# Kernel tuning notes

Hardware: AMD Instinct MI355X
Metric: run time of the kernel (lower is better)

The kernel has to match this reference:

```python
import jax, jax.numpy as jnp
import numpy as np

K_FRAC = 0.5  # matches init kwarg k


def setup_inputs() -> dict:
    key = jax.random.key(0)
    g = jax.random.normal(key, (16, 2048, 2048), dtype=jnp.float32)
    return {"g": g}


def reference(g):
    # k = int(N * k_frac): number of SMALLEST entries per row to zero out
    N = g.shape[-1]
    k = int(N * K_FRAC)
    g2 = g.reshape(-1, N)                       # [R, N]
    # indices of the k smallest values per row (topk of -g)
    _, idx = jax.lax.top_k(-g2, k)              # [R, k] int32
    rows = jnp.arange(g2.shape[0])[:, None]     # [R, 1]
    t = g2.at[rows, idx].set(0.0)               # scatter zeros at bottom-k positions
    return t.reshape(g.shape)
```

## Files before the change

### kernel.cpp

```cpp
#include <hip/hip_runtime.h>

#define ROW_N 2048
#define ROW_K 1024
#define NSUB 4
#define HPAD 264
#define WH   (NSUB * HPAD)
#define WSTRIDE (WH + 4)

__device__ __forceinline__ void wfence() {
    asm volatile("s_waitcnt lgkmcnt(0)" ::: "memory");
}

__device__ __forceinline__ unsigned f2key(float x) {
    unsigned u = __float_as_uint(x);
    return u ^ ((unsigned)((int)u >> 31) | 0x80000000u);
}
__device__ __forceinline__ float key2f(unsigned k) {
    unsigned u = (k & 0x80000000u) ? (k ^ 0x80000000u) : ~k;
    return __uint_as_float(u);
}

__global__ __launch_bounds__(256)
void ktakes_kernel(const float* __restrict__ g, float* __restrict__ out) {
    const int tid  = threadIdx.x;
    const int wave = tid >> 6;
    const int lane = tid & 63;
    const int row  = blockIdx.x * 4 + wave;

    __shared__ unsigned H[4 * WSTRIDE];
    unsigned* hw   = H + wave * WSTRIDE;
    unsigned* hsub = hw + (lane & (NSUB - 1)) * HPAD;

    const float4* g4 = reinterpret_cast<const float4*>(g + (size_t)row * ROW_N);
    float4*       o4 = reinterpret_cast<float4*>(out + (size_t)row * ROW_N);

    unsigned k[32];
#pragma unroll
    for (int j = 0; j < 8; ++j) {
        float4 v = g4[j * 64 + lane];
        k[4*j+0] = f2key(v.x); k[4*j+1] = f2key(v.y);
        k[4*j+2] = f2key(v.z); k[4*j+3] = f2key(v.w);
    }

    unsigned prefix = 0;
    int rank = ROW_K - 1;
    int cnteq = 0;

#pragma unroll
    for (int r = 0; r < 4; ++r) {
        const int shift = 24 - 8 * r;

#pragma unroll
        for (int i = 0; i < 17; ++i) {
            int idx = i * 64 + lane;
            if (idx < WH) hw[idx] = 0;
        }
        wfence();

        if (r == 0) {
#pragma unroll
            for (int c = 0; c < 32; ++c)
                atomicAdd(&hsub[k[c] >> 24], 1u);
        } else {
            const int hs = shift + 8;
#pragma unroll
            for (int c = 0; c < 32; ++c)
                if (((k[c] ^ prefix) >> hs) == 0)
                    atomicAdd(&hsub[(k[c] >> shift) & 255u], 1u);
        }
        wfence();

        uint4 h0 = *reinterpret_cast<const uint4*>(&hw[0 * HPAD + 4 * lane]);
        uint4 h1 = *reinterpret_cast<const uint4*>(&hw[1 * HPAD + 4 * lane]);
        uint4 h2 = *reinterpret_cast<const uint4*>(&hw[2 * HPAD + 4 * lane]);
        uint4 h3 = *reinterpret_cast<const uint4*>(&hw[3 * HPAD + 4 * lane]);
        unsigned b0 = h0.x + h1.x + h2.x + h3.x;
        unsigned b1 = h0.y + h1.y + h2.y + h3.y;
        unsigned b2 = h0.z + h1.z + h2.z + h3.z;
        unsigned b3 = h0.w + h1.w + h2.w + h3.w;
        wfence();

        unsigned s4 = b0 + b1 + b2 + b3;
        unsigned incl = s4;
#pragma unroll
        for (int off = 1; off < 64; off <<= 1) {
            unsigned n = __shfl_up(incl, off, 64);
            if (lane >= off) incl += n;
        }
        int excl = (int)(incl - s4);
        bool found = (rank >= excl) && (rank < (int)incl);

        int rr = rank - excl;
        unsigned d = 4 * lane;
        unsigned beq = b0;
        if (found) {
            if (rr >= (int)b0) { rr -= (int)b0; d++; beq = b1;
                if (rr >= (int)b1) { rr -= (int)b1; d++; beq = b2;
                    if (rr >= (int)b2) { rr -= (int)b2; d++; beq = b3; } } }
        }
        unsigned long long bal = __ballot(found);
        int src = __builtin_ctzll(bal);
        d     = (unsigned)__shfl((int)d, src, 64);
        rr    = __shfl(rr, src, 64);
        beq   = (unsigned)__shfl((int)beq, src, 64);

        prefix |= d << shift;
        rank  = rr;
        cnteq = (int)beq;
    }

    const unsigned Kth = prefix;
    const int m = rank + 1;

    unsigned zm = 0;
    if (cnteq == m) {
#pragma unroll
        for (int c = 0; c < 32; ++c)
            if (k[c] <= Kth) zm |= 1u << c;
    } else {
        int base = 0;
#pragma unroll
        for (int j = 0; j < 8; ++j) {
            int eqmask = 0, e = 0;
#pragma unroll
            for (int c = 0; c < 4; ++c) {
                bool q = (k[4*j+c] == Kth);
                eqmask |= (int)q << c; e += (int)q;
            }
            int incl = e;
#pragma unroll
            for (int off = 1; off < 64; off <<= 1) {
                int n = __shfl_up(incl, off, 64);
                if (lane >= off) incl += n;
            }
            int excl = incl - e;
            int tot = __shfl(incl, 63, 64);
            int pos = base + excl;
#pragma unroll
            for (int c = 0; c < 4; ++c) {
                if (eqmask & (1 << c)) {
                    if (pos < m) zm |= 1u << (4*j+c);
                    pos++;
                }
            }
            base += tot;
        }
#pragma unroll
        for (int c = 0; c < 32; ++c)
            if (k[c] < Kth) zm |= 1u << c;
    }

#pragma unroll
    for (int j = 0; j < 8; ++j) {
        float4 v;
        v.x = (zm >> (4*j+0)) & 1u ? 0.0f : key2f(k[4*j+0]);
        v.y = (zm >> (4*j+1)) & 1u ? 0.0f : key2f(k[4*j+1]);
        v.z = (zm >> (4*j+2)) & 1u ? 0.0f : key2f(k[4*j+2]);
        v.w = (zm >> (4*j+3)) & 1u ? 0.0f : key2f(k[4*j+3]);
        o4[j * 64 + lane] = v;
    }
}

extern "C" void kernel_launch(void* const* d_in, const int* in_sizes, int n_in,
                              void* d_out, int out_size, void* d_ws, size_t ws_size,
                              hipStream_t stream) {
    const float* g = (const float*)d_in[0];
    float* out = (float*)d_out;
    const int rows = in_sizes[0] / ROW_N;
    hipLaunchKernelGGL(ktakes_kernel, dim3(rows / 4), dim3(256), 0, stream, g, out);
}
```

Measured before the change: 433.0 us.

## Use single histogram for later radix passes, pack shuffle results, raise occupancy

New measurement: 450.2 us. +4.0%, slower.

```diff
diff --git a/kernel.cpp b/kernel.cpp
--- a/kernel.cpp
+++ b/kernel.cpp
@@ -20,7 +20,37 @@
     return __uint_as_float(u);
 }
 
-__global__ __launch_bounds__(256)
+__device__ __forceinline__ void scan_pick(unsigned b0, unsigned b1, unsigned b2,
+                                          unsigned b3, int lane, int rank_in,
+                                          unsigned& digit, int& rank_out,
+                                          int& cnteq_out) {
+    unsigned s4 = b0 + b1 + b2 + b3;
+    unsigned incl = s4;
+#pragma unroll
+    for (int off = 1; off < 64; off <<= 1) {
+        unsigned n = __shfl_up(incl, off, 64);
+        if (lane >= off) incl += n;
+    }
+    int excl = (int)(incl - s4);
+    bool found = (rank_in >= excl) && (rank_in < (int)incl);
+    int rr = rank_in - excl;
+    unsigned d = 4 * lane;
+    unsigned beq = b0;
+    if (found) {
+        if (rr >= (int)b0) { rr -= (int)b0; d++; beq = b1;
+            if (rr >= (int)b1) { rr -= (int)b1; d++; beq = b2;
+                if (rr >= (int)b2) { rr -= (int)b2; d++; beq = b3; } } }
+    }
+    unsigned pack = (d << 24) | (beq << 12) | (unsigned)rr;
+    unsigned long long bal = __ballot(found);
+    int src = __builtin_ctzll(bal);
+    pack = (unsigned)__shfl((int)pack, src, 64);
+    digit = pack >> 24;
+    cnteq_out = (int)((pack >> 12) & 0xfffu);
+    rank_out = (int)(pack & 0xfffu);
+}
+
+__global__ __launch_bounds__(256, 8)
 void ktakes_kernel(const float* __restrict__ g, float* __restrict__ out) {
     const int tid  = threadIdx.x;
     const int wave = tid >> 6;
@@ -29,6 +59,7 @@
 
     __shared__ unsigned H[4 * WSTRIDE];
     unsigned* hw   = H + wave * WSTRIDE;
+    uint4*    hw4  = reinterpret_cast<uint4*>(hw);
     unsigned* hsub = hw + (lane & (NSUB - 1)) * HPAD;
 
     const float4* g4 = reinterpret_cast<const float4*>(g + (size_t)row * ROW_N);
@@ -42,71 +73,48 @@
         k[4*j+2] = f2key(v.z); k[4*j+3] = f2key(v.w);
     }
 
-    unsigned prefix = 0;
-    int rank = ROW_K - 1;
-    int cnteq = 0;
+    const uint4 z4 = {0u, 0u, 0u, 0u};
+    unsigned prefix;
+    int rank, cnteq;
+
+    {
+#pragma unroll
+        for (int i = 0; i < 4; ++i) hw4[i * 64 + lane] = z4;
+        if (lane < 32) hw[1024 + lane] = 0;
+        wfence();
+#pragma unroll
+        for (int c = 0; c < 32; ++c)
+            atomicAdd(&hsub[k[c] >> 24], 1u);
+        wfence();
+        unsigned b0 = 0, b1 = 0, b2 = 0, b3 = 0;
+#pragma unroll
+        for (int s = 0; s < NSUB; ++s) {
+            uint4 h = *reinterpret_cast<const uint4*>(&hw[s * HPAD + 4 * lane]);
+            b0 += h.x; b1 += h.y; b2 += h.z; b3 += h.w;
+        }
+        wfence();
+        unsigned d;
+        scan_pick(b0, b1, b2, b3, lane, ROW_K - 1, d, rank, cnteq);
+        prefix = d << 24;
+    }
 
 #pragma unroll
-    for (int r = 0; r < 4; ++r) {
+    for (int r = 1; r < 4; ++r) {
         const int shift = 24 - 8 * r;
+        const int hs = shift + 8;
 
+        hw4[lane] = z4;
+        wfence();
 #pragma unroll
-        for (int i = 0; i < 17; ++i) {
-            int idx = i * 64 + lane;
-            if (idx < WH) hw[idx] = 0;
-        }
+        for (int c = 0; c < 32; ++c)
+            if (((k[c] ^ prefix) >> hs) == 0)
+                atomicAdd(&hw[(k[c] >> shift) & 255u], 1u);
         wfence();
-
-        if (r == 0) {
-#pragma unroll
-            for (int c = 0; c < 32; ++c)
-                atomicAdd(&hsub[k[c] >> 24], 1u);
-        } else {
-            const int hs = shift + 8;
-#pragma unroll
-            for (int c = 0; c < 32; ++c)
-                if (((k[c] ^ prefix) >> hs) == 0)
-                    atomicAdd(&hsub[(k[c] >> shift) & 255u], 1u);
-        }
+        uint4 h = hw4[lane];
         wfence();
-
-        uint4 h0 = *reinterpret_cast<const uint4*>(&hw[0 * HPAD + 4 * lane]);
-        uint4 h1 = *reinterpret_cast<const uint4*>(&hw[1 * HPAD + 4 * lane]);
-        uint4 h2 = *reinterpret_cast<const uint4*>(&hw[2 * HPAD + 4 * lane]);
-        uint4 h3 = *reinterpret_cast<const uint4*>(&hw[3 * HPAD + 4 * lane]);
-        unsigned b0 = h0.x + h1.x + h2.x + h3.x;
-        unsigned b1 = h0.y + h1.y + h2.y + h3.y;
-        unsigned b2 = h0.z + h1.z + h2.z + h3.z;
-        unsigned b3 = h0.w + h1.w + h2.w + h3.w;
-        wfence();
-
-        unsigned s4 = b0 + b1 + b2 + b3;
-        unsigned incl = s4;
-#pragma unroll
-        for (int off = 1; off < 64; off <<= 1) {
-            unsigned n = __shfl_up(incl, off, 64);
-            if (lane >= off) incl += n;
-        }
-        int excl = (int)(incl - s4);
-        bool found = (rank >= excl) && (rank < (int)incl);
-
-        int rr = rank - excl;
-        unsigned d = 4 * lane;
-        unsigned beq = b0;
-        if (found) {
-            if (rr >= (int)b0) { rr -= (int)b0; d++; beq = b1;
-                if (rr >= (int)b1) { rr -= (int)b1; d++; beq = b2;
-                    if (rr >= (int)b2) { rr -= (int)b2; d++; beq = b3; } } }
-        }
-        unsigned long long bal = __ballot(found);
-        int src = __builtin_ctzll(bal);
-        d     = (unsigned)__shfl((int)d, src, 64);
-        rr    = __shfl(rr, src, 64);
-        beq   = (unsigned)__shfl((int)beq, src, 64);
-
+        unsigned d;
+        scan_pick(h.x, h.y, h.z, h.w, lane, rank, d, rank, cnteq);
         prefix |= d << shift;
-        rank  = rr;
-        cnteq = (int)beq;
     }
 
     const unsigned Kth = prefix;
```
